# Kernel tuning notes

Hardware: AMD Instinct MI355X
Metric: run time of the kernel (lower is better)

## Reference

```python
import jax, jax.numpy as jnp
import numpy as np


def log_g(x):
    # log of g(x) = x+0.5 if x>=0 else sigmoid(x)
    return jnp.where(x >= 0, jnp.log(jax.nn.relu(x) + 0.5), -jax.nn.softplus(-x))


def setup_inputs() -> dict:
    key = jax.random.key(0)
    B, T, D, H = 8, 4096, 1024, 1024
    ks = jax.random.split(key, 7)
    s = 1.0 / np.sqrt(D)
    return {
        "x": jax.random.normal(ks[0], (B, T, D), dtype=jnp.float32),
        "h0": jnp.zeros((B, 1, H), dtype=jnp.float32),
        "W_f": jax.random.uniform(ks[1], (H, D), jnp.float32, -s, s),
        "b_f": jax.random.uniform(ks[2], (H,), jnp.float32, -s, s),
        "W_i": jax.random.uniform(ks[3], (H, D), jnp.float32, -s, s),
        "b_i": jax.random.uniform(ks[4], (H,), jnp.float32, -s, s),
        "W_h": jax.random.uniform(ks[5], (H, D), jnp.float32, -s, s),
        "b_h": jax.random.uniform(ks[6], (H,), jnp.float32, -s, s),
    }


def reference(x, h0, W_f, b_f, W_i, b_i, W_h, b_h):
    # gate pre-activations: [B, T, H]
    zf = jnp.einsum("btd,hd->bth", x, W_f) + b_f
    zi = jnp.einsum("btd,hd->bth", x, W_i) + b_i
    zh = jnp.einsum("btd,hd->bth", x, W_h) + b_h
    diff = jax.nn.softplus(-zf) - jax.nn.softplus(-zi)
    log_f = -jax.nn.softplus(diff)        # log f'_t
    log_i = -jax.nn.softplus(-diff)       # log i'_t
    log_values = jnp.concatenate([log_g(h0), log_i + log_g(zh)], axis=1)  # [B, T+1, H]
    # parallel scan in log space
    a_star = jnp.pad(jnp.cumsum(log_f, axis=1), ((0, 0), (1, 0), (0, 0)))  # [B, T+1, H]
    log_h = a_star + jax.lax.cumlogsumexp(log_values - a_star, axis=1)
    return jnp.exp(log_h)[:, 1:]  # [B, T, H]
```

## Files before the change

kernel.cpp:

```cpp
#include <hip/hip_runtime.h>
#include <hip/hip_bf16.h>
#include <stdint.h>
#include <stddef.h>

#define B_ 8
#define T_ 4096
#define D_ 1024
#define H_ 1024
#define M_ (B_*T_)
#define K_ 1024
#define CHUNK 64
#define NCHUNK 64
#define NWGF ((M_/128)*(H_/128))

typedef __attribute__((ext_vector_type(8))) __bf16 bf16v8;
typedef __attribute__((ext_vector_type(4))) float f32x4;
typedef __attribute__((ext_vector_type(8))) unsigned short u16x8;

#define QA  0
#define QBF 16384
#define QBI 32768
#define QBH 49152
#define SLOT 65536
#define LDS_BYTES 131072

#define FENCE() asm volatile("" ::: "memory")
#define SBAR()  __builtin_amdgcn_s_barrier()

__device__ __forceinline__ unsigned short f2bf(float f) {
  union { float f; unsigned u; } x; x.f = f;
  return (unsigned short)((x.u + 0x7fffu + ((x.u >> 16) & 1u)) >> 16);
}

__global__ __launch_bounds__(256) void cvt_x(const float* __restrict__ src,
                                             unsigned short* __restrict__ dst) {
  int i = blockIdx.x * 256 + threadIdx.x;
  const float4* s = (const float4*)src;
  float4 a = s[i*2], b = s[i*2+1];
  u16x8 o;
  o[0]=f2bf(a.x); o[1]=f2bf(a.y); o[2]=f2bf(a.z); o[3]=f2bf(a.w);
  o[4]=f2bf(b.x); o[5]=f2bf(b.y); o[6]=f2bf(b.z); o[7]=f2bf(b.w);
  *(u16x8*)(dst + (size_t)i*8) = o;
}

__global__ __launch_bounds__(256) void cvt_w(const float* __restrict__ w0,
                                             const float* __restrict__ w1,
                                             const float* __restrict__ w2,
                                             unsigned short* __restrict__ dst) {
  int i = blockIdx.x * 256 + threadIdx.x;
  int seg = i >> 17;
  int off = i & 131071;
  const float* src = (seg == 0) ? w0 : (seg == 1) ? w1 : w2;
  const float4* s = (const float4*)src;
  float4 a = s[off*2], b = s[off*2+1];
  u16x8 o;
  o[0]=f2bf(a.x); o[1]=f2bf(a.y); o[2]=f2bf(a.z); o[3]=f2bf(a.w);
  o[4]=f2bf(b.x); o[5]=f2bf(b.y); o[6]=f2bf(b.z); o[7]=f2bf(b.w);
  *(u16x8*)(dst + (size_t)i*8) = o;
}

__device__ __forceinline__ void stage_mat(char* lbase, const unsigned short* gbase,
                                          int k0, int tid) {
  #pragma unroll
  for (int l = 0; l < 2; ++l) {
    int o = tid*16 + l*8192;
    int row = o >> 7, cb = o & 127;
    int scb = cb ^ ((row & 7) << 4);
    const unsigned short* g = gbase + (size_t)row * K_ + k0 + (scb >> 1);
    __builtin_amdgcn_global_load_lds((const __attribute__((address_space(1))) void*)g,
        (__attribute__((address_space(3))) void*)(lbase + o), 16, 0, 0);
  }
}

__device__ __forceinline__ bf16v8 ldsRd(const char* base, int rr, int cb) {
  return *(const bf16v8*)(base + rr*128 + (cb ^ ((rr & 7) << 4)));
}

__device__ __forceinline__ void gate_eval(float vzf, float vzi, float vzh,
                                          float& f, float& v) {
  float spf = fmaxf(-vzf, 0.f) + __logf(1.f + __expf(-fabsf(vzf)));
  float spi = fmaxf(-vzi, 0.f) + __logf(1.f + __expf(-fabsf(vzi)));
  float d   = spf - spi;
  float l1  = __logf(1.f + __expf(-fabsf(d)));
  f = __expf(-(fmaxf(d, 0.f) + l1));
  float iv = __expf(-(fmaxf(-d, 0.f) + l1));
  float gv = (vzh >= 0.f) ? (vzh + 0.5f) : 1.f/(1.f + __expf(-vzh));
  v = iv * gv;
}

__global__ __launch_bounds__(512, 2) void gemm_fused(
    const unsigned short* __restrict__ Abf,
    const unsigned short* __restrict__ Wc,
    const float* __restrict__ bf_, const float* __restrict__ bi_,
    const float* __restrict__ bh_,
    uint32_t* __restrict__ fv)
{
  extern __shared__ char smem[];
  int tid = threadIdx.x;
  int bid = blockIdx.x;
  int swz = (bid & 7) * (NWGF/8) + (bid >> 3);
  int tn = swz & 7, tm = swz >> 3;
  int m0 = tm*128, n0 = tn*128;
  int lane = tid & 63, wid = tid >> 6;
  int wm = wid >> 2, wn = wid & 3;
  int lr = lane & 15, lhi = lane >> 4;
  int cbL = lhi * 16;

  const unsigned short* Ag  = Abf + (size_t)m0 * K_;
  const unsigned short* BFg = Wc + (size_t)n0 * K_;
  const unsigned short* BIg = Wc + (size_t)(H_ + n0) * K_;
  const unsigned short* BHg = Wc + (size_t)(2*H_ + n0) * K_;

  f32x4 accF[4][2] = {}, accI[4][2] = {}, accH[4][2] = {};
  bf16v8 af[4][2], bF[2][2], bI[2][2], bH[2][2];

  stage_mat(smem + QA,  Ag,  0, tid);
  stage_mat(smem + QBF, BFg, 0, tid);
  stage_mat(smem + QBI, BIg, 0, tid);
  stage_mat(smem + QBH, BHg, 0, tid);
  asm volatile("s_waitcnt vmcnt(4)" ::: "memory");
  SBAR(); FENCE();

  for (int t = 0; t < 16; ++t) {
    char* rd = smem + (t & 1)*SLOT;
    char* wr = smem + ((t & 1) ^ 1)*SLOT;
    int k1 = (t+1)*64;
    bool st = (t < 15);
    #pragma unroll
    for (int i = 0; i < 4; ++i)
      #pragma unroll
      for (int kk = 0; kk < 2; ++kk)
        af[i][kk] = ldsRd(rd + QA, wm*64 + i*16 + lr, kk*64 + cbL);
    #pragma unroll
    for (int j = 0; j < 2; ++j)
      #pragma unroll
      for (int kk = 0; kk < 2; ++kk)
        bF[j][kk] = ldsRd(rd + QBF, wn*32 + j*16 + lr, kk*64 + cbL);
    if (st) { stage_mat(wr + QA, Ag, k1, tid); stage_mat(wr + QBF, BFg, k1, tid); }
    FENCE();
    __builtin_amdgcn_s_setprio(1);
    #pragma unroll
    for (int i = 0; i < 4; ++i)
      #pragma unroll
      for (int j = 0; j < 2; ++j)
        #pragma unroll
        for (int kk = 0; kk < 2; ++kk)
          accF[i][j] = __builtin_amdgcn_mfma_f32_16x16x32_bf16(af[i][kk], bF[j][kk], accF[i][j], 0, 0, 0);
    __builtin_amdgcn_s_setprio(0);
    FENCE();
    if (st) { asm volatile("s_waitcnt vmcnt(6)" ::: "memory"); }
    else    { asm volatile("s_waitcnt vmcnt(2)" ::: "memory"); }
    SBAR(); FENCE();
    #pragma unroll
    for (int j = 0; j < 2; ++j)
      #pragma unroll
      for (int kk = 0; kk < 2; ++kk)
        bI[j][kk] = ldsRd(rd + QBI, wn*32 + j*16 + lr, kk*64 + cbL);
    if (st) stage_mat(wr + QBI, BIg, k1, tid);
    FENCE();
    __builtin_amdgcn_s_setprio(1);
    #pragma unroll
    for (int i = 0; i < 4; ++i)
      #pragma unroll
      for (int j = 0; j < 2; ++j)
        #pragma unroll
        for (int kk = 0; kk < 2; ++kk)
          accI[i][j] = __builtin_amdgcn_mfma_f32_16x16x32_bf16(af[i][kk], bI[j][kk], accI[i][j], 0, 0, 0);
    __builtin_amdgcn_s_setprio(0);
    FENCE();
    if (st) { asm volatile("s_waitcnt vmcnt(6)" ::: "memory"); }
    else    { asm volatile("s_waitcnt vmcnt(0)" ::: "memory"); }
    SBAR(); FENCE();
    #pragma unroll
    for (int j = 0; j < 2; ++j)
      #pragma unroll
      for (int kk = 0; kk < 2; ++kk)
        bH[j][kk] = ldsRd(rd + QBH, wn*32 + j*16 + lr, kk*64 + cbL);
    if (st) stage_mat(wr + QBH, BHg, k1, tid);
    FENCE();
    __builtin_amdgcn_s_setprio(1);
    #pragma unroll
    for (int i = 0; i < 4; ++i)
      #pragma unroll
      for (int j = 0; j < 2; ++j)
        #pragma unroll
        for (int kk = 0; kk < 2; ++kk)
          accH[i][j] = __builtin_amdgcn_mfma_f32_16x16x32_bf16(af[i][kk], bH[j][kk], accH[i][j], 0, 0, 0);
    __builtin_amdgcn_s_setprio(0);
    if (st) { asm volatile("s_waitcnt vmcnt(4)" ::: "memory"); SBAR(); FENCE(); }
  }

  float bfv[2], biv[2], bhv[2];
  #pragma unroll
  for (int j = 0; j < 2; ++j) {
    int col = n0 + wn*32 + j*16 + lr;
    bfv[j] = bf_[col]; biv[j] = bi_[col]; bhv[j] = bh_[col];
  }
  #pragma unroll
  for (int i = 0; i < 4; ++i)
    #pragma unroll
    for (int j = 0; j < 2; ++j) {
      int col = n0 + wn*32 + j*16 + lr;
      int row0 = m0 + wm*64 + i*16 + lhi*4;
      #pragma unroll
      for (int r = 0; r < 4; ++r) {
        float f, v;
        gate_eval(accF[i][j][r] + bfv[j], accI[i][j][r] + biv[j],
                  accH[i][j][r] + bhv[j], f, v);
        fv[(size_t)(row0 + r)*H_ + col] =
            (uint32_t)f2bf(f) | ((uint32_t)f2bf(v) << 16);
      }
    }
}

__global__ __launch_bounds__(256) void scan_phaseA(
    const uint32_t* __restrict__ fv,
    float* __restrict__ Aw, float* __restrict__ Sw)
{
  int blk = blockIdx.x;
  int c = blk & 63, b = blk >> 6;
  int h4 = threadIdx.x * 4;
  size_t base = ((size_t)b*T_ + (size_t)c*CHUNK)*H_ + h4;
  float Ap[4] = {1.f,1.f,1.f,1.f}, S[4] = {0.f,0.f,0.f,0.f};
  for (int t = 0; t < CHUNK; ++t) {
    uint4 pk = *(const uint4*)(fv + base + (size_t)t*H_);
    uint32_t w[4] = {pk.x, pk.y, pk.z, pk.w};
    #pragma unroll
    for (int u = 0; u < 4; ++u) {
      union { uint32_t u; float f; } cf, cv;
      cf.u = (w[u] & 0xffffu) << 16;
      cv.u = w[u] & 0xffff0000u;
      S[u] = fmaf(cf.f, S[u], cv.f);
      Ap[u] *= cf.f;
    }
  }
  size_t widx = ((size_t)b*NCHUNK + c)*H_ + h4;
  *(float4*)(Aw + widx) = make_float4(Ap[0], Ap[1], Ap[2], Ap[3]);
  *(float4*)(Sw + widx) = make_float4(S[0], S[1], S[2], S[3]);
}

__global__ __launch_bounds__(256) void scan_phaseB(
    const float* __restrict__ Aw, const float* __restrict__ Sw,
    const float* __restrict__ h0, float* __restrict__ Cw)
{
  int i = blockIdx.x*256 + threadIdx.x;
  int b = i >> 8;
  int h4 = (i & 255) * 4;
  float4 x0 = *(const float4*)(h0 + (size_t)b*H_ + h4);
  float run[4];
  const float* px = (const float*)&x0;
  #pragma unroll
  for (int u = 0; u < 4; ++u)
    run[u] = (px[u] >= 0.f) ? (px[u] + 0.5f) : 1.f/(1.f + __expf(-px[u]));
  for (int c = 0; c < NCHUNK; ++c) {
    size_t idx = ((size_t)b*NCHUNK + c)*H_ + h4;
    *(float4*)(Cw + idx) = make_float4(run[0], run[1], run[2], run[3]);
    float4 av = *(const float4*)(Aw + idx);
    float4 sv = *(const float4*)(Sw + idx);
    const float* pa = (const float*)&av;
    const float* ps = (const float*)&sv;
    #pragma unroll
    for (int u = 0; u < 4; ++u) run[u] = fmaf(pa[u], run[u], ps[u]);
  }
}

__global__ __launch_bounds__(256) void scan_phaseC(
    const uint32_t* __restrict__ fv, const float* __restrict__ Cw,
    float* __restrict__ out)
{
  int blk = blockIdx.x;
  int c = blk & 63, b = blk >> 6;
  int h4 = threadIdx.x * 4;
  float4 cw = *(const float4*)(Cw + ((size_t)b*NCHUNK + c)*H_ + h4);
  float hh[4];
  const float* pc = (const float*)&cw;
  #pragma unroll
  for (int u = 0; u < 4; ++u) hh[u] = pc[u];
  size_t base = ((size_t)b*T_ + (size_t)c*CHUNK)*H_ + h4;
  for (int t = 0; t < CHUNK; ++t) {
    size_t idx = base + (size_t)t*H_;
    uint4 pk = *(const uint4*)(fv + idx);
    uint32_t w[4] = {pk.x, pk.y, pk.z, pk.w};
    #pragma unroll
    for (int u = 0; u < 4; ++u) {
      union { uint32_t u; float f; } cf, cv;
      cf.u = (w[u] & 0xffffu) << 16;
      cv.u = w[u] & 0xffff0000u;
      hh[u] = fmaf(cf.f, hh[u], cv.f);
    }
    *(float4*)(out + idx) = make_float4(hh[0], hh[1], hh[2], hh[3]);
  }
}

extern "C" void kernel_launch(void* const* d_in, const int* in_sizes, int n_in,
                              void* d_out, int out_size, void* d_ws, size_t ws_size,
                              hipStream_t stream) {
  const float* x   = (const float*)d_in[0];
  const float* h0  = (const float*)d_in[1];
  const float* W_f = (const float*)d_in[2];
  const float* b_f = (const float*)d_in[3];
  const float* W_i = (const float*)d_in[4];
  const float* b_i = (const float*)d_in[5];
  const float* W_h = (const float*)d_in[6];
  const float* b_h = (const float*)d_in[7];
  float* out = (float*)d_out;

  char* ws = (char*)d_ws;
  unsigned short* xb = (unsigned short*)ws;
  unsigned short* Wc = (unsigned short*)(ws + (size_t)M_*K_*2);
  uint32_t* fv = (uint32_t*)(ws + (size_t)M_*K_*2 + (size_t)3*H_*K_*2);
  float* Aw = (float*)(fv + (size_t)M_*H_);
  float* Sw = Aw + (size_t)B_*NCHUNK*H_;
  float* Cw = Sw + (size_t)B_*NCHUNK*H_;

  (void)hipFuncSetAttribute((const void*)gemm_fused,
      hipFuncAttributeMaxDynamicSharedMemorySize, LDS_BYTES);

  cvt_x<<<M_*K_/8/256, 256, 0, stream>>>(x, xb);
  cvt_w<<<3*H_*K_/8/256, 256, 0, stream>>>(W_f, W_i, W_h, Wc);

  gemm_fused<<<NWGF, 512, LDS_BYTES, stream>>>(xb, Wc, b_f, b_i, b_h, fv);

  scan_phaseA<<<B_*NCHUNK, 256, 0, stream>>>(fv, Aw, Sw);
  scan_phaseB<<<B_*H_/4/256, 256, 0, stream>>>(Aw, Sw, h0, Cw);
  scan_phaseC<<<B_*NCHUNK, 256, 0, stream>>>(fv, Cw, out);
}
```

Before: 567.5 us.

## Precompute staging pointers, unroll GEMM k-loop by two, halve scan chunk size

Three changes. The GEMM main loop is manually unrolled by two with fixed double-buffer slots, and the global-to-LDS staging addresses are precomputed once as pointers that are bumped each step, so the per-iteration address arithmetic and branches go away. The scan chunk size is halved to 32, doubling the number of chunks and therefore the parallelism in phases A and C, at the cost of a longer serial phase B. Phases A and C also prefetch the next row's packed values one iteration ahead to hide load latency.

```diff
diff --git a/kernel.cpp b/kernel.cpp
--- a/kernel.cpp
+++ b/kernel.cpp
@@ -9,8 +9,8 @@
 #define H_ 1024
 #define M_ (B_*T_)
 #define K_ 1024
-#define CHUNK 64
-#define NCHUNK 64
+#define CHUNK 32
+#define NCHUNK 128
 #define NWGF ((M_/128)*(H_/128))
 
 typedef __attribute__((ext_vector_type(8))) __bf16 bf16v8;
@@ -26,6 +26,9 @@
 
 #define FENCE() asm volatile("" ::: "memory")
 #define SBAR()  __builtin_amdgcn_s_barrier()
+#define STG(p, d) __builtin_amdgcn_global_load_lds(                        \
+    (const __attribute__((address_space(1))) void*)(p),                    \
+    (__attribute__((address_space(3))) void*)(d), 16, 0, 0)
 
 __device__ __forceinline__ unsigned short f2bf(float f) {
   union { float f; unsigned u; } x; x.f = f;
@@ -59,21 +62,41 @@
   *(u16x8*)(dst + (size_t)i*8) = o;
 }
 
-__device__ __forceinline__ void stage_mat(char* lbase, const unsigned short* gbase,
-                                          int k0, int tid) {
-  #pragma unroll
-  for (int l = 0; l < 2; ++l) {
-    int o = tid*16 + l*8192;
-    int row = o >> 7, cb = o & 127;
-    int scb = cb ^ ((row & 7) << 4);
-    const unsigned short* g = gbase + (size_t)row * K_ + k0 + (scb >> 1);
-    __builtin_amdgcn_global_load_lds((const __attribute__((address_space(1))) void*)g,
-        (__attribute__((address_space(3))) void*)(lbase + o), 16, 0, 0);
-  }
-}
-
-__device__ __forceinline__ bf16v8 ldsRd(const char* base, int rr, int cb) {
-  return *(const bf16v8*)(base + rr*128 + (cb ^ ((rr & 7) << 4)));
+__device__ __forceinline__ void rdA8(const char* rbase, int wm, int lr, int cbL,
+                                     bf16v8 af[4][2]) {
+  #pragma unroll
+  for (int i = 0; i < 4; ++i)
+    #pragma unroll
+    for (int kk = 0; kk < 2; ++kk) {
+      int rr = wm*64 + i*16 + lr;
+      int cb = kk*64 + cbL;
+      af[i][kk] = *(const bf16v8*)(rbase + rr*128 + (cb ^ ((rr & 7) << 4)));
+    }
+}
+
+__device__ __forceinline__ void rdB4(const char* rbase, int wn, int lr, int cbL,
+                                     bf16v8 b[2][2]) {
+  #pragma unroll
+  for (int j = 0; j < 2; ++j)
+    #pragma unroll
+    for (int kk = 0; kk < 2; ++kk) {
+      int rr = wn*32 + j*16 + lr;
+      int cb = kk*64 + cbL;
+      b[j][kk] = *(const bf16v8*)(rbase + rr*128 + (cb ^ ((rr & 7) << 4)));
+    }
+}
+
+__device__ __forceinline__ void mm16(f32x4 acc[4][2], bf16v8 af[4][2],
+                                     bf16v8 b[2][2]) {
+  __builtin_amdgcn_s_setprio(1);
+  #pragma unroll
+  for (int i = 0; i < 4; ++i)
+    #pragma unroll
+    for (int j = 0; j < 2; ++j)
+      #pragma unroll
+      for (int kk = 0; kk < 2; ++kk)
+        acc[i][j] = __builtin_amdgcn_mfma_f32_16x16x32_bf16(af[i][kk], b[j][kk], acc[i][j], 0, 0, 0);
+  __builtin_amdgcn_s_setprio(0);
 }
 
 __device__ __forceinline__ void gate_eval(float vzf, float vzi, float vzh,
@@ -87,6 +110,28 @@
   float gv = (vzh >= 0.f) ? (vzh + 0.5f) : 1.f/(1.f + __expf(-vzh));
   v = iv * gv;
 }
+
+#define STEP_FULL(RD, SOFF, KB)                                              \
+  {                                                                          \
+    const char* rd = smem + (RD)*SLOT;                                       \
+    rdA8(rd + QA,  wm, lr, cbL, af);                                         \
+    rdB4(rd + QBF, wn, lr, cbL, bF);                                         \
+    STG(pA0 + (KB), dA0 + (SOFF)); STG(pA1 + (KB), dA1 + (SOFF));            \
+    STG(pF0 + (KB), dF0 + (SOFF)); STG(pF1 + (KB), dF1 + (SOFF));            \
+    FENCE();                                                                 \
+    mm16(accF, af, bF);                                                      \
+    asm volatile("s_waitcnt vmcnt(6)" ::: "memory"); SBAR(); FENCE();        \
+    rdB4(rd + QBI, wn, lr, cbL, bI);                                         \
+    STG(pI0 + (KB), dI0 + (SOFF)); STG(pI1 + (KB), dI1 + (SOFF));            \
+    FENCE();                                                                 \
+    mm16(accI, af, bI);                                                      \
+    asm volatile("s_waitcnt vmcnt(6)" ::: "memory"); SBAR(); FENCE();        \
+    rdB4(rd + QBH, wn, lr, cbL, bH);                                         \
+    STG(pH0 + (KB), dH0 + (SOFF)); STG(pH1 + (KB), dH1 + (SOFF));            \
+    FENCE();                                                                 \
+    mm16(accH, af, bH);                                                      \
+    asm volatile("s_waitcnt vmcnt(4)" ::: "memory"); SBAR(); FENCE();        \
+  }
 
 __global__ __launch_bounds__(512, 2) void gemm_fused(
     const unsigned short* __restrict__ Abf,
@@ -111,83 +156,57 @@
   const unsigned short* BIg = Wc + (size_t)(H_ + n0) * K_;
   const unsigned short* BHg = Wc + (size_t)(2*H_ + n0) * K_;
 
+  int o0 = tid*16, o1 = o0 + 8192;
+  int r0 = o0 >> 7, c0 = o0 & 127;
+  int r1 = o1 >> 7, c1 = o1 & 127;
+  size_t lo0 = (size_t)r0*K_ + (size_t)((c0 ^ ((r0 & 7) << 4)) >> 1);
+  size_t lo1 = (size_t)r1*K_ + (size_t)((c1 ^ ((r1 & 7) << 4)) >> 1);
+  const char* pA0 = (const char*)(Ag  + lo0);
+  const char* pA1 = (const char*)(Ag  + lo1);
+  const char* pF0 = (const char*)(BFg + lo0);
+  const char* pF1 = (const char*)(BFg + lo1);
+  const char* pI0 = (const char*)(BIg + lo0);
+  const char* pI1 = (const char*)(BIg + lo1);
+  const char* pH0 = (const char*)(BHg + lo0);
+  const char* pH1 = (const char*)(BHg + lo1);
+  char* dA0 = smem + QA  + o0;  char* dA1 = smem + QA  + o1;
+  char* dF0 = smem + QBF + o0;  char* dF1 = smem + QBF + o1;
+  char* dI0 = smem + QBI + o0;  char* dI1 = smem + QBI + o1;
+  char* dH0 = smem + QBH + o0;  char* dH1 = smem + QBH + o1;
+
   f32x4 accF[4][2] = {}, accI[4][2] = {}, accH[4][2] = {};
   bf16v8 af[4][2], bF[2][2], bI[2][2], bH[2][2];
 
-  stage_mat(smem + QA,  Ag,  0, tid);
-  stage_mat(smem + QBF, BFg, 0, tid);
-  stage_mat(smem + QBI, BIg, 0, tid);
-  stage_mat(smem + QBH, BHg, 0, tid);
+  STG(pA0, dA0); STG(pA1, dA1);
+  STG(pF0, dF0); STG(pF1, dF1);
+  STG(pI0, dI0); STG(pI1, dI1);
+  STG(pH0, dH0); STG(pH1, dH1);
+  pA0 += 128; pA1 += 128; pF0 += 128; pF1 += 128;
+  pI0 += 128; pI1 += 128; pH0 += 128; pH1 += 128;
   asm volatile("s_waitcnt vmcnt(4)" ::: "memory");
   SBAR(); FENCE();
 
-  for (int t = 0; t < 16; ++t) {
-    char* rd = smem + (t & 1)*SLOT;
-    char* wr = smem + ((t & 1) ^ 1)*SLOT;
-    int k1 = (t+1)*64;
-    bool st = (t < 15);
-    #pragma unroll
-    for (int i = 0; i < 4; ++i)
-      #pragma unroll
-      for (int kk = 0; kk < 2; ++kk)
-        af[i][kk] = ldsRd(rd + QA, wm*64 + i*16 + lr, kk*64 + cbL);
-    #pragma unroll
-    for (int j = 0; j < 2; ++j)
-      #pragma unroll
-      for (int kk = 0; kk < 2; ++kk)
-        bF[j][kk] = ldsRd(rd + QBF, wn*32 + j*16 + lr, kk*64 + cbL);
-    if (st) { stage_mat(wr + QA, Ag, k1, tid); stage_mat(wr + QBF, BFg, k1, tid); }
+  for (int tt = 0; tt < 7; ++tt) {
+    STEP_FULL(0, SLOT, 0)
+    STEP_FULL(1, 0, 128)
+    pA0 += 256; pA1 += 256; pF0 += 256; pF1 += 256;
+    pI0 += 256; pI1 += 256; pH0 += 256; pH1 += 256;
+  }
+  STEP_FULL(0, SLOT, 0)
+  {
+    const char* rd = smem + SLOT;
+    rdA8(rd + QA,  wm, lr, cbL, af);
+    rdB4(rd + QBF, wn, lr, cbL, bF);
     FENCE();
-    __builtin_amdgcn_s_setprio(1);
-    #pragma unroll
-    for (int i = 0; i < 4; ++i)
-      #pragma unroll
-      for (int j = 0; j < 2; ++j)
-        #pragma unroll
-        for (int kk = 0; kk < 2; ++kk)
-          accF[i][j] = __builtin_amdgcn_mfma_f32_16x16x32_bf16(af[i][kk], bF[j][kk], accF[i][j], 0, 0, 0);
-    __builtin_amdgcn_s_setprio(0);
+    mm16(accF, af, bF);
+    asm volatile("s_waitcnt vmcnt(2)" ::: "memory"); SBAR(); FENCE();
+    rdB4(rd + QBI, wn, lr, cbL, bI);
     FENCE();
-    if (st) { asm volatile("s_waitcnt vmcnt(6)" ::: "memory"); }
-    else    { asm volatile("s_waitcnt vmcnt(2)" ::: "memory"); }
-    SBAR(); FENCE();
-    #pragma unroll
-    for (int j = 0; j < 2; ++j)
-      #pragma unroll
-      for (int kk = 0; kk < 2; ++kk)
-        bI[j][kk] = ldsRd(rd + QBI, wn*32 + j*16 + lr, kk*64 + cbL);
-    if (st) stage_mat(wr + QBI, BIg, k1, tid);
+    mm16(accI, af, bI);
+    asm volatile("s_waitcnt vmcnt(0)" ::: "memory"); SBAR(); FENCE();
+    rdB4(rd + QBH, wn, lr, cbL, bH);
     FENCE();
-    __builtin_amdgcn_s_setprio(1);
-    #pragma unroll
-    for (int i = 0; i < 4; ++i)
-      #pragma unroll
-      for (int j = 0; j < 2; ++j)
-        #pragma unroll
-        for (int kk = 0; kk < 2; ++kk)
-          accI[i][j] = __builtin_amdgcn_mfma_f32_16x16x32_bf16(af[i][kk], bI[j][kk], accI[i][j], 0, 0, 0);
-    __builtin_amdgcn_s_setprio(0);
-    FENCE();
-    if (st) { asm volatile("s_waitcnt vmcnt(6)" ::: "memory"); }
-    else    { asm volatile("s_waitcnt vmcnt(0)" ::: "memory"); }
-    SBAR(); FENCE();
-    #pragma unroll
-    for (int j = 0; j < 2; ++j)
-      #pragma unroll
-      for (int kk = 0; kk < 2; ++kk)
-        bH[j][kk] = ldsRd(rd + QBH, wn*32 + j*16 + lr, kk*64 + cbL);
-    if (st) stage_mat(wr + QBH, BHg, k1, tid);
-    FENCE();
-    __builtin_amdgcn_s_setprio(1);
-    #pragma unroll
-    for (int i = 0; i < 4; ++i)
-      #pragma unroll
-      for (int j = 0; j < 2; ++j)
-        #pragma unroll
-        for (int kk = 0; kk < 2; ++kk)
-          accH[i][j] = __builtin_amdgcn_mfma_f32_16x16x32_bf16(af[i][kk], bH[j][kk], accH[i][j], 0, 0, 0);
-    __builtin_amdgcn_s_setprio(0);
-    if (st) { asm volatile("s_waitcnt vmcnt(4)" ::: "memory"); SBAR(); FENCE(); }
+    mm16(accH, af, bH);
   }
 
   float bfv[2], biv[2], bhv[2];
@@ -218,12 +237,14 @@
     float* __restrict__ Aw, float* __restrict__ Sw)
 {
   int blk = blockIdx.x;
-  int c = blk & 63, b = blk >> 6;
+  int c = blk & 127, b = blk >> 7;
   int h4 = threadIdx.x * 4;
   size_t base = ((size_t)b*T_ + (size_t)c*CHUNK)*H_ + h4;
   float Ap[4] = {1.f,1.f,1.f,1.f}, S[4] = {0.f,0.f,0.f,0.f};
+  uint4 pk = *(const uint4*)(fv + base);
   for (int t = 0; t < CHUNK; ++t) {
-    uint4 pk = *(const uint4*)(fv + base + (size_t)t*H_);
+    uint4 nx = pk;
+    if (t + 1 < CHUNK) nx = *(const uint4*)(fv + base + (size_t)(t+1)*H_);
     uint32_t w[4] = {pk.x, pk.y, pk.z, pk.w};
     #pragma unroll
     for (int u = 0; u < 4; ++u) {
@@ -233,6 +254,7 @@
       S[u] = fmaf(cf.f, S[u], cv.f);
       Ap[u] *= cf.f;
     }
+    pk = nx;
   }
   size_t widx = ((size_t)b*NCHUNK + c)*H_ + h4;
   *(float4*)(Aw + widx) = make_float4(Ap[0], Ap[1], Ap[2], Ap[3]);
@@ -269,7 +291,7 @@
     float* __restrict__ out)
 {
   int blk = blockIdx.x;
-  int c = blk & 63, b = blk >> 6;
+  int c = blk & 127, b = blk >> 7;
   int h4 = threadIdx.x * 4;
   float4 cw = *(const float4*)(Cw + ((size_t)b*NCHUNK + c)*H_ + h4);
   float hh[4];
@@ -277,9 +299,10 @@
   #pragma unroll
   for (int u = 0; u < 4; ++u) hh[u] = pc[u];
   size_t base = ((size_t)b*T_ + (size_t)c*CHUNK)*H_ + h4;
+  uint4 pk = *(const uint4*)(fv + base);
   for (int t = 0; t < CHUNK; ++t) {
-    size_t idx = base + (size_t)t*H_;
-    uint4 pk = *(const uint4*)(fv + idx);
+    uint4 nx = pk;
+    if (t + 1 < CHUNK) nx = *(const uint4*)(fv + base + (size_t)(t+1)*H_);
     uint32_t w[4] = {pk.x, pk.y, pk.z, pk.w};
     #pragma unroll
     for (int u = 0; u < 4; ++u) {
@@ -288,7 +311,8 @@
       cv.u = w[u] & 0xffff0000u;
       hh[u] = fmaf(cf.f, hh[u], cv.f);
     }
-    *(float4*)(out + idx) = make_float4(hh[0], hh[1], hh[2], hh[3]);
+    *(float4*)(out + base + (size_t)t*H_) = make_float4(hh[0], hh[1], hh[2], hh[3]);
+    pk = nx;
   }
 }
 
```

Result: slower. 588.5 us (+3.7%).
